# Kernel tuning notes

Measured on AMD Instinct MI355X. Metric: run time of the kernel, lower is better.

Reference implementation:

```python
import jax, jax.numpy as jnp
import numpy as np

B, N, DIM, SUB = 4, 96, 128, 8


def _lin_init(key, fan_in, fan_out):
    k1, k2 = jax.random.split(key)
    bound = 1.0 / np.sqrt(fan_in)
    W = jax.random.uniform(k1, (fan_in, fan_out), jnp.float32, -bound, bound)
    b = jax.random.uniform(k2, (fan_out,), jnp.float32, -bound, bound)
    return W, b


def setup_inputs() -> dict:
    key = jax.random.key(0)
    ks = jax.random.split(key, 6)
    node_emb = jax.random.normal(ks[0], (B * N, DIM), jnp.float32)
    path_emb = jax.random.normal(ks[1], (B, N, N, DIM), jnp.float32)
    Wn, bn = _lin_init(ks[2], DIM, SUB)          # node_proj
    We, be = _lin_init(ks[3], DIM, SUB)          # edge_proj
    Wt, bt = _lin_init(ks[4], 6 * SUB, SUB)      # triplet_func Linear
    Wo, bo = _lin_init(ks[5], SUB, DIM)          # out_func Linear
    return {"node_emb": node_emb, "path_emb": path_emb,
            "Wn": Wn, "bn": bn, "We": We, "be": be,
            "Wt": Wt, "bt": bt, "Wo": Wo, "bo": bo}


def reference(node_emb, path_emb, Wn, bn, We, be, Wt, bt, Wo, bo):
    b, n = path_emb.shape[0], path_emb.shape[1]
    s = Wn.shape[1]
    # projections
    pn = (node_emb @ Wn + bn).reshape(b, n, s)       # (b, n, s)
    pe = path_emb @ We + be                          # (b, n, n, s)
    # Split the 6*s -> s triplet linear by input block so we never materialize
    # the (b,n,n,n,6s) concat: cat order is [n_i, n_j, n_k, e_ik, e_kj, e_ij].
    W1, W2, W3, W4, W5, W6 = jnp.split(Wt, 6, axis=0)
    ti = pn @ W1                                     # indexed by i -> (b, i, s)
    tj = pn @ W2                                     # indexed by j
    tk = pn @ W3                                     # indexed by k
    e_ik = pe @ W4                                   # (b, i, k, s)
    e_kj = pe @ W5                                   # (b, k, j, s)
    e_ij = pe @ W6                                   # (b, i, j, s)
    X = e_ik + tk[:, None, :, :]                     # (b, i, k, s)
    Y = jnp.transpose(e_kj, (0, 2, 1, 3))            # (b, j, k, s)
    Z = e_ij + ti[:, :, None, :] + tj[:, None, :, :] + bt  # (b, i, j, s)
    # (b, i, j, k, s) pre-activation, ReLU, then max over k
    scores = jax.nn.relu(X[:, :, None, :, :] + Y[:, None, :, :, :] + Z[:, :, :, None, :])
    t_ij = jnp.max(scores, axis=-2)                  # (b, i, j, s)
    out = jax.nn.relu(t_ij @ Wo + bo)                # (b, i, j, dim)
    return out
```

## Files before the change

### kernel.cpp

```cpp
#include <hip/hip_runtime.h>

#define B_   4
#define N_   96
#define DIM_ 128
#define PB   (N_*N_)
#define NPOS (B_*PB)

#define OFF_WEFF 0
#define OFF_CALL 3072
#define OFF_TN   3104
#define OFF_X    12320
#define OFF_Y    307232
#define OFF_Z    602144
#define OFF_T    897056

__global__ __launch_bounds__(256) void k0_prep(
    const float* __restrict__ node, const float* __restrict__ Wn,
    const float* __restrict__ bn,   const float* __restrict__ We,
    const float* __restrict__ be,   const float* __restrict__ Wt,
    const float* __restrict__ bt,   float* __restrict__ ws) {
  const int tid = threadIdx.x;
  if (blockIdx.x == 32) {
    for (int idx = tid; idx < 24*128; idx += 256) {
      int t = idx >> 7, d = idx & 127;
      int g = t >> 3, s = t & 7;
      float v = 0.f;
#pragma unroll
      for (int u = 0; u < 8; ++u) v += We[d*8+u] * Wt[((3+g)*8+u)*8 + s];
      ws[OFF_WEFF + t*128 + d] = v;
    }
    if (tid < 24) {
      int g = tid >> 3, s = tid & 7;
      float v = 0.f;
#pragma unroll
      for (int u = 0; u < 8; ++u) v += be[u] * Wt[((3+g)*8+u)*8 + s];
      if (g == 2) v += bt[s];
      ws[OFF_CALL + tid] = v;
    }
  } else {
    __shared__ float ww[24*130];
    __shared__ float nl[12*130];
    for (int idx = tid; idx < 3*128*8; idx += 256) {
      int g = idx >> 10, rem = idx & 1023;
      int d = rem >> 3, s = rem & 7;
      float v = 0.f;
#pragma unroll
      for (int u = 0; u < 8; ++u) v += Wn[d*8+u] * Wt[(g*8+u)*8 + s];
      ww[(g*8+s)*130 + d] = v;
    }
    const int p0 = blockIdx.x * 12;
    for (int f = tid; f < 12*128; f += 256) {
      int pr = f >> 7, d = f & 127;
      nl[pr*130 + d] = node[(p0+pr)*DIM_ + d];
    }
    __syncthreads();
    for (int idx = tid; idx < 12*24; idx += 256) {
      int pr = idx / 24, t = idx - pr*24;
      int g = t >> 3, s = t & 7;
      float v = 0.f;
#pragma unroll
      for (int u = 0; u < 8; ++u) v += bn[u] * Wt[(g*8+u)*8 + s];
      const float* a = nl + pr*130;
      const float* w = ww + (g*8+s)*130;
#pragma unroll 8
      for (int d = 0; d < 128; ++d) v += a[d] * w[d];
      ws[OFF_TN + (p0+pr)*24 + t] = v;
    }
  }
}

__global__ __launch_bounds__(256) void k1_proj(
    const float* __restrict__ P, const float* __restrict__ wsc,
    float* __restrict__ ws) {
  __shared__ float lp[64*132];
  __shared__ float tnl[96*24];
  const int tid = threadIdx.x;
  const int blk = blockIdx.x;
  const int b   = blk / 144;
  const int p0  = (blk - b*144) * 64;
  const float4* Pg = (const float4*)(P + ((size_t)b*PB + p0) * DIM_);
#pragma unroll
  for (int k = 0; k < 8; ++k) {
    int f = tid + k*256;
    float4 v = Pg[f];
    int l = f >> 5, dd = f & 31;
    *(float4*)(lp + l*132 + dd*4) = v;
  }
  const float4* Tg4 = (const float4*)(wsc + OFF_TN + b*(96*24));
  for (int f = tid; f < 576; f += 256) ((float4*)tnl)[f] = Tg4[f];
  __syncthreads();

  const int w    = __builtin_amdgcn_readfirstlane((int)(threadIdx.x >> 6));
  const int lane = tid & 63;
  const int t0   = w * 6;
  const int pos  = p0 + lane;
  const int r    = pos / 96;
  const int c    = pos - r*96;
  const float* pa = lp + lane*132;
  const float* wp = wsc + OFF_WEFF + t0*128;
  float acc[6] = {0.f,0.f,0.f,0.f,0.f,0.f};
#pragma unroll 4
  for (int d = 0; d < 128; d += 4) {
    float4 va = *(const float4*)(pa + d);
#pragma unroll
    for (int tt = 0; tt < 6; ++tt) {
      float4 wv = *(const float4*)(wp + tt*128 + d);
      acc[tt] += va.x*wv.x + va.y*wv.y + va.z*wv.z + va.w*wv.w;
    }
  }
  float* Xs = ws + OFF_X; float* Ys = ws + OFF_Y; float* Zs = ws + OFF_Z;
#pragma unroll
  for (int tt = 0; tt < 6; ++tt) {
    int t = t0 + tt;
    float val = acc[tt] + wsc[OFF_CALL + t];
    if (t < 8) {
      val += tnl[c*24 + 16 + t];
      Xs[((b*8+t)*N_ + r)*N_ + c] = val;
    } else if (t < 16) {
      int s = t - 8;
      Ys[((b*8+s)*N_ + r)*N_ + c] = val;
    } else {
      int s = t - 16;
      val += tnl[r*24 + s] + tnl[c*24 + 8 + s];
      Zs[((b*8+s)*N_ + r)*N_ + c] = val;
    }
  }
}

__global__ __launch_bounds__(256) void k2_maxplus(
    const float* __restrict__ wsc, float* __restrict__ ws) {
  __shared__ float xs [24*100];
  __shared__ float ysl[24*100];
  __shared__ float zl [24*24];
  __shared__ float red[3*64*9];
  const int tid = threadIdx.x;
  const int bs = blockIdx.x >> 4;
  const int it = (blockIdx.x >> 2) & 3;
  const int jt = blockIdx.x & 3;
  const float* Xg = wsc + OFF_X + (bs*N_ + it*24)*N_;
  const float* Yg = wsc + OFF_Y + (size_t)bs*N_*N_ + jt*24;
  const float* Zg = wsc + OFF_Z + (bs*N_ + it*24)*N_ + jt*24;
  for (int f = tid; f < 576; f += 256) {
    int row = f / 24, kk = f - row*24;
    *(float4*)(xs + row*100 + kk*4) = *(const float4*)(Xg + row*N_ + kk*4);
  }
  for (int f = tid; f < 576; f += 256) {
    int k = f / 6, jq = f - k*6;
    float4 v = *(const float4*)(Yg + k*N_ + jq*4);
    ysl[(jq*4+0)*100 + k] = v.x;
    ysl[(jq*4+1)*100 + k] = v.y;
    ysl[(jq*4+2)*100 + k] = v.z;
    ysl[(jq*4+3)*100 + k] = v.w;
  }
  for (int f = tid; f < 144; f += 256) {
    int row = f / 6, kk = f - row*6;
    *(float4*)(zl + row*24 + kk*4) = *(const float4*)(Zg + row*N_ + kk*4);
  }
  __syncthreads();
  const int kc = tid >> 6, lane = tid & 63;
  const int ig = lane >> 3, jg = lane & 7;
  float z[3][3], m[3][3];
#pragma unroll
  for (int di = 0; di < 3; ++di)
#pragma unroll
    for (int dj = 0; dj < 3; ++dj) {
      z[di][dj] = zl[(ig*3+di)*24 + jg*3 + dj];
      m[di][dj] = 0.f;
    }
  const float* xb = xs  + (ig*3)*100 + kc*24;
  const float* yb = ysl + (jg*3)*100 + kc*24;
#pragma unroll 4
  for (int k = 0; k < 24; k += 2) {
    float2 xv[3], yv[3];
#pragma unroll
    for (int d = 0; d < 3; ++d) xv[d] = *(const float2*)(xb + d*100 + k);
#pragma unroll
    for (int d = 0; d < 3; ++d) yv[d] = *(const float2*)(yb + d*100 + k);
#pragma unroll
    for (int di = 0; di < 3; ++di)
#pragma unroll
      for (int dj = 0; dj < 3; ++dj) {
        float v0 = xv[di].x + yv[dj].x + z[di][dj];
        float v1 = xv[di].y + yv[dj].y + z[di][dj];
        m[di][dj] = fmaxf(m[di][dj], fmaxf(v0, 0.f));
        m[di][dj] = fmaxf(m[di][dj], fmaxf(v1, 0.f));
      }
  }
  if (kc > 0) {
    float* rp = red + ((kc-1)*64 + lane)*9;
#pragma unroll
    for (int q = 0; q < 9; ++q) rp[q] = m[q/3][q%3];
  }
  __syncthreads();
  if (kc == 0) {
#pragma unroll
    for (int kk = 0; kk < 3; ++kk) {
      const float* rp = red + (kk*64 + lane)*9;
#pragma unroll
      for (int q = 0; q < 9; ++q) m[q/3][q%3] = fmaxf(m[q/3][q%3], rp[q]);
    }
    float* Tg = ws + OFF_T + (bs*N_ + it*24 + ig*3)*N_ + jt*24 + jg*3;
#pragma unroll
    for (int di = 0; di < 3; ++di)
#pragma unroll
      for (int dj = 0; dj < 3; ++dj)
        Tg[di*N_ + dj] = m[di][dj];
  }
}

__global__ __launch_bounds__(256) void k3_out(
    const float* __restrict__ wsc, const float* __restrict__ Wo,
    const float* __restrict__ bo,  float* __restrict__ out) {
  __shared__ float ts[8*72];
  const int tid = threadIdx.x;
  const int blk = blockIdx.x;
  const int b   = blk >> 7;
  const int off = (blk & 127) * 72;
  const float* Tg = wsc + OFF_T + b*8*PB + off;
  for (int f = tid; f < 144; f += 256) {
    int s = f / 18, kk = f - s*18;
    *(float4*)(ts + s*72 + kk*4) = *(const float4*)(Tg + s*PB + kk*4);
  }
  __syncthreads();
  const int dq = tid & 31;
  const int q  = tid >> 5;
  float wo[8][4];
#pragma unroll
  for (int s = 0; s < 8; ++s) {
    float4 wv = *(const float4*)(Wo + s*DIM_ + dq*4);
    wo[s][0]=wv.x; wo[s][1]=wv.y; wo[s][2]=wv.z; wo[s][3]=wv.w;
  }
  float4 bv = *(const float4*)(bo + dq*4);
  const size_t pbase = (size_t)b*PB + off;
  for (int p = 0; p < 9; ++p) {
    int pp = q*9 + p;
    float a0 = bv.x, a1 = bv.y, a2 = bv.z, a3 = bv.w;
#pragma unroll
    for (int s = 0; s < 8; ++s) {
      float tv = ts[s*72 + pp];
      a0 += tv*wo[s][0]; a1 += tv*wo[s][1];
      a2 += tv*wo[s][2]; a3 += tv*wo[s][3];
    }
    float4 o = make_float4(fmaxf(a0,0.f), fmaxf(a1,0.f),
                           fmaxf(a2,0.f), fmaxf(a3,0.f));
    *(float4*)(out + (pbase + pp)*DIM_ + dq*4) = o;
  }
}

extern "C" void kernel_launch(void* const* d_in, const int* in_sizes, int n_in,
                              void* d_out, int out_size, void* d_ws, size_t ws_size,
                              hipStream_t stream) {
  const float* node = (const float*)d_in[0];
  const float* path = (const float*)d_in[1];
  const float* Wn   = (const float*)d_in[2];
  const float* bn   = (const float*)d_in[3];
  const float* We   = (const float*)d_in[4];
  const float* be   = (const float*)d_in[5];
  const float* Wt   = (const float*)d_in[6];
  const float* bt   = (const float*)d_in[7];
  const float* Wo   = (const float*)d_in[8];
  const float* bo   = (const float*)d_in[9];
  float* ws  = (float*)d_ws;
  float* out = (float*)d_out;

  k0_prep   <<<dim3(33),  dim3(256), 0, stream>>>(node, Wn, bn, We, be, Wt, bt, ws);
  k1_proj   <<<dim3(576), dim3(256), 0, stream>>>(path, ws, ws);
  k2_maxplus<<<dim3(512), dim3(256), 0, stream>>>(ws, ws);
  k3_out    <<<dim3(512), dim3(256), 0, stream>>>(ws, Wo, bo, out);
}
```

Baseline: 115.8 us.

## Fuse four kernel launches into one cooperative kernel with grid syncs

Merges the prep, projection, max-plus and output stages into a single cooperative kernel of 576 blocks that separates stages with grid.sync(). The aim is to remove the launch overhead and inter-kernel gaps between the four launches. If the cooperative launch fails, it falls back to the original four launches. The trade-off is the cost of grid-wide barriers, idle blocks in stages that use fewer blocks, and a 43KB static shared allocation that may limit occupancy.

```diff
diff --git a/kernel.cpp b/kernel.cpp
--- a/kernel.cpp
+++ b/kernel.cpp
@@ -1,10 +1,12 @@
 #include <hip/hip_runtime.h>
+#include <hip/hip_cooperative_groups.h>
+
+namespace cg = cooperative_groups;
 
 #define B_   4
 #define N_   96
 #define DIM_ 128
 #define PB   (N_*N_)
-#define NPOS (B_*PB)
 
 #define OFF_WEFF 0
 #define OFF_CALL 3072
@@ -247,6 +249,240 @@
   }
 }
 
+__global__ __launch_bounds__(256, 3) void fused_all(
+    const float* __restrict__ node, const float* __restrict__ P,
+    const float* __restrict__ Wn,   const float* __restrict__ bn,
+    const float* __restrict__ We,   const float* __restrict__ be,
+    const float* __restrict__ Wt,   const float* __restrict__ bt,
+    const float* __restrict__ Wo,   const float* __restrict__ bo,
+    float* __restrict__ ws,         float* __restrict__ out) {
+  cg::grid_group grid = cg::this_grid();
+  __shared__ float smem[10752];
+  const int tid = threadIdx.x;
+  const int blk = blockIdx.x;
+
+  if (blk < 33) {
+    if (blk == 32) {
+      for (int idx = tid; idx < 24*128; idx += 256) {
+        int t = idx >> 7, d = idx & 127;
+        int g = t >> 3, s = t & 7;
+        float v = 0.f;
+#pragma unroll
+        for (int u = 0; u < 8; ++u) v += We[d*8+u] * Wt[((3+g)*8+u)*8 + s];
+        ws[OFF_WEFF + t*128 + d] = v;
+      }
+      if (tid < 24) {
+        int g = tid >> 3, s = tid & 7;
+        float v = 0.f;
+#pragma unroll
+        for (int u = 0; u < 8; ++u) v += be[u] * Wt[((3+g)*8+u)*8 + s];
+        if (g == 2) v += bt[s];
+        ws[OFF_CALL + tid] = v;
+      }
+    } else {
+      float* ww = smem;
+      float* nl = smem + 3120;
+      for (int idx = tid; idx < 3*128*8; idx += 256) {
+        int g = idx >> 10, rem = idx & 1023;
+        int d = rem >> 3, s = rem & 7;
+        float v = 0.f;
+#pragma unroll
+        for (int u = 0; u < 8; ++u) v += Wn[d*8+u] * Wt[(g*8+u)*8 + s];
+        ww[(g*8+s)*130 + d] = v;
+      }
+      const int p0 = blk * 12;
+      for (int f = tid; f < 12*128; f += 256) {
+        int pr = f >> 7, d = f & 127;
+        nl[pr*130 + d] = node[(p0+pr)*DIM_ + d];
+      }
+      __syncthreads();
+      for (int idx = tid; idx < 12*24; idx += 256) {
+        int pr = idx / 24, t = idx - pr*24;
+        int g = t >> 3, s = t & 7;
+        float v = 0.f;
+#pragma unroll
+        for (int u = 0; u < 8; ++u) v += bn[u] * Wt[(g*8+u)*8 + s];
+        const float* a = nl + pr*130;
+        const float* w = ww + (g*8+s)*130;
+#pragma unroll 8
+        for (int d = 0; d < 128; ++d) v += a[d] * w[d];
+        ws[OFF_TN + (p0+pr)*24 + t] = v;
+      }
+    }
+  }
+  grid.sync();
+
+  {
+    float* lp  = smem;
+    float* tnl = smem + 8448;
+    const int b  = blk / 144;
+    const int p0 = (blk - b*144) * 64;
+    const float4* Pg = (const float4*)(P + ((size_t)b*PB + p0) * DIM_);
+#pragma unroll
+    for (int k = 0; k < 8; ++k) {
+      int f = tid + k*256;
+      float4 v = Pg[f];
+      int l = f >> 5, dd = f & 31;
+      *(float4*)(lp + l*132 + dd*4) = v;
+    }
+    const float4* Tg4 = (const float4*)(ws + OFF_TN + b*(96*24));
+    for (int f = tid; f < 576; f += 256) ((float4*)tnl)[f] = Tg4[f];
+    __syncthreads();
+
+    const int w    = __builtin_amdgcn_readfirstlane((int)(threadIdx.x >> 6));
+    const int lane = tid & 63;
+    const int t0   = w * 6;
+    const int pos  = p0 + lane;
+    const int r    = pos / 96;
+    const int c    = pos - r*96;
+    const float* pa = lp + lane*132;
+    const float* wp = ws + OFF_WEFF + t0*128;
+    float acc[6] = {0.f,0.f,0.f,0.f,0.f,0.f};
+#pragma unroll 4
+    for (int d = 0; d < 128; d += 4) {
+      float4 va = *(const float4*)(pa + d);
+#pragma unroll
+      for (int tt = 0; tt < 6; ++tt) {
+        float4 wv = *(const float4*)(wp + tt*128 + d);
+        acc[tt] += va.x*wv.x + va.y*wv.y + va.z*wv.z + va.w*wv.w;
+      }
+    }
+    float* Xs = ws + OFF_X; float* Ys = ws + OFF_Y; float* Zs = ws + OFF_Z;
+#pragma unroll
+    for (int tt = 0; tt < 6; ++tt) {
+      int t = t0 + tt;
+      float val = acc[tt] + ws[OFF_CALL + t];
+      if (t < 8) {
+        val += tnl[c*24 + 16 + t];
+        Xs[((b*8+t)*N_ + r)*N_ + c] = val;
+      } else if (t < 16) {
+        int s = t - 8;
+        Ys[((b*8+s)*N_ + r)*N_ + c] = val;
+      } else {
+        int s = t - 16;
+        val += tnl[r*24 + s] + tnl[c*24 + 8 + s];
+        Zs[((b*8+s)*N_ + r)*N_ + c] = val;
+      }
+    }
+  }
+  grid.sync();
+
+  if (blk < 512) {
+    float* xs  = smem;
+    float* ysl = smem + 2400;
+    float* zl  = smem + 4800;
+    float* red = smem + 5376;
+    const int bs = blk >> 4;
+    const int it = (blk >> 2) & 3;
+    const int jt = blk & 3;
+    const float* Xg = ws + OFF_X + (bs*N_ + it*24)*N_;
+    const float* Yg = ws + OFF_Y + (size_t)bs*N_*N_ + jt*24;
+    const float* Zg = ws + OFF_Z + (bs*N_ + it*24)*N_ + jt*24;
+    for (int f = tid; f < 576; f += 256) {
+      int row = f / 24, kk = f - row*24;
+      *(float4*)(xs + row*100 + kk*4) = *(const float4*)(Xg + row*N_ + kk*4);
+    }
+    for (int f = tid; f < 576; f += 256) {
+      int k = f / 6, jq = f - k*6;
+      float4 v = *(const float4*)(Yg + k*N_ + jq*4);
+      ysl[(jq*4+0)*100 + k] = v.x;
+      ysl[(jq*4+1)*100 + k] = v.y;
+      ysl[(jq*4+2)*100 + k] = v.z;
+      ysl[(jq*4+3)*100 + k] = v.w;
+    }
+    for (int f = tid; f < 144; f += 256) {
+      int row = f / 6, kk = f - row*6;
+      *(float4*)(zl + row*24 + kk*4) = *(const float4*)(Zg + row*N_ + kk*4);
+    }
+    __syncthreads();
+    const int kc = tid >> 6, lane = tid & 63;
+    const int ig = lane >> 3, jg = lane & 7;
+    float z[3][3], m[3][3];
+#pragma unroll
+    for (int di = 0; di < 3; ++di)
+#pragma unroll
+      for (int dj = 0; dj < 3; ++dj) {
+        z[di][dj] = zl[(ig*3+di)*24 + jg*3 + dj];
+        m[di][dj] = 0.f;
+      }
+    const float* xb = xs  + (ig*3)*100 + kc*24;
+    const float* yb = ysl + (jg*3)*100 + kc*24;
+#pragma unroll 4
+    for (int k = 0; k < 24; k += 2) {
+      float2 xv[3], yv[3];
+#pragma unroll
+      for (int d = 0; d < 3; ++d) xv[d] = *(const float2*)(xb + d*100 + k);
+#pragma unroll
+      for (int d = 0; d < 3; ++d) yv[d] = *(const float2*)(yb + d*100 + k);
+#pragma unroll
+      for (int di = 0; di < 3; ++di)
+#pragma unroll
+        for (int dj = 0; dj < 3; ++dj) {
+          float v0 = xv[di].x + yv[dj].x + z[di][dj];
+          float v1 = xv[di].y + yv[dj].y + z[di][dj];
+          m[di][dj] = fmaxf(m[di][dj], fmaxf(v0, 0.f));
+          m[di][dj] = fmaxf(m[di][dj], fmaxf(v1, 0.f));
+        }
+    }
+    if (kc > 0) {
+      float* rp = red + ((kc-1)*64 + lane)*9;
+#pragma unroll
+      for (int q = 0; q < 9; ++q) rp[q] = m[q/3][q%3];
+    }
+    __syncthreads();
+    if (kc == 0) {
+#pragma unroll
+      for (int kk = 0; kk < 3; ++kk) {
+        const float* rp = red + (kk*64 + lane)*9;
+#pragma unroll
+        for (int q = 0; q < 9; ++q) m[q/3][q%3] = fmaxf(m[q/3][q%3], rp[q]);
+      }
+      float* Tg = ws + OFF_T + (bs*N_ + it*24 + ig*3)*N_ + jt*24 + jg*3;
+#pragma unroll
+      for (int di = 0; di < 3; ++di)
+#pragma unroll
+        for (int dj = 0; dj < 3; ++dj)
+          Tg[di*N_ + dj] = m[di][dj];
+    }
+  }
+  grid.sync();
+
+  if (blk < 512) {
+    float* ts = smem;
+    const int b   = blk >> 7;
+    const int off = (blk & 127) * 72;
+    const float* Tg = ws + OFF_T + b*8*PB + off;
+    for (int f = tid; f < 144; f += 256) {
+      int s = f / 18, kk = f - s*18;
+      *(float4*)(ts + s*72 + kk*4) = *(const float4*)(Tg + s*PB + kk*4);
+    }
+    __syncthreads();
+    const int dq = tid & 31;
+    const int q  = tid >> 5;
+    float wo[8][4];
+#pragma unroll
+    for (int s = 0; s < 8; ++s) {
+      float4 wv = *(const float4*)(Wo + s*DIM_ + dq*4);
+      wo[s][0]=wv.x; wo[s][1]=wv.y; wo[s][2]=wv.z; wo[s][3]=wv.w;
+    }
+    float4 bv = *(const float4*)(bo + dq*4);
+    const size_t pbase = (size_t)b*PB + off;
+    for (int p = 0; p < 9; ++p) {
+      int pp = q*9 + p;
+      float a0 = bv.x, a1 = bv.y, a2 = bv.z, a3 = bv.w;
+#pragma unroll
+      for (int s = 0; s < 8; ++s) {
+        float tv = ts[s*72 + pp];
+        a0 += tv*wo[s][0]; a1 += tv*wo[s][1];
+        a2 += tv*wo[s][2]; a3 += tv*wo[s][3];
+      }
+      float4 o = make_float4(fmaxf(a0,0.f), fmaxf(a1,0.f),
+                             fmaxf(a2,0.f), fmaxf(a3,0.f));
+      *(float4*)(out + (pbase + pp)*DIM_ + dq*4) = o;
+    }
+  }
+}
+
 extern "C" void kernel_launch(void* const* d_in, const int* in_sizes, int n_in,
                               void* d_out, int out_size, void* d_ws, size_t ws_size,
                               hipStream_t stream) {
@@ -263,8 +499,16 @@
   float* ws  = (float*)d_ws;
   float* out = (float*)d_out;
 
-  k0_prep   <<<dim3(33),  dim3(256), 0, stream>>>(node, Wn, bn, We, be, Wt, bt, ws);
-  k1_proj   <<<dim3(576), dim3(256), 0, stream>>>(path, ws, ws);
-  k2_maxplus<<<dim3(512), dim3(256), 0, stream>>>(ws, ws);
-  k3_out    <<<dim3(512), dim3(256), 0, stream>>>(ws, Wo, bo, out);
+  void* args[] = {(void*)&node, (void*)&path, (void*)&Wn, (void*)&bn,
+                  (void*)&We,   (void*)&be,   (void*)&Wt, (void*)&bt,
+                  (void*)&Wo,   (void*)&bo,   (void*)&ws, (void*)&out};
+  hipError_t err = hipLaunchCooperativeKernel((const void*)fused_all,
+                                              dim3(576), dim3(256),
+                                              args, 0, stream);
+  if (err != hipSuccess) {
+    k0_prep   <<<dim3(33),  dim3(256), 0, stream>>>(node, Wn, bn, We, be, Wt, bt, ws);
+    k1_proj   <<<dim3(576), dim3(256), 0, stream>>>(path, ws, ws);
+    k2_maxplus<<<dim3(512), dim3(256), 0, stream>>>(ws, ws);
+    k3_out    <<<dim3(512), dim3(256), 0, stream>>>(ws, Wo, bo, out);
+  }
 }
```

Measured after the change: 312.3 us. +169.6%, slower.
